# Kernel optimization log

Measured on AMD Instinct MI355X. Metric: run time of the kernel, lower is better.

The kernel has to match this reference:

```python
import jax, jax.numpy as jnp
import numpy as np

EPS_BN = 1e-5
EPS_NORM = 1e-12


def _l2norm_c(x):
    # F.normalize over channel dim (dim=1) of [n, d, h, w]
    n = jnp.sqrt(jnp.sum(x * x, axis=1, keepdims=True))
    return x / jnp.maximum(n, EPS_NORM)


def setup_inputs() -> dict:
    key = jax.random.key(0)
    ks = jax.random.split(key, 8)
    g, p, d, h, w = 64, 64, 512, 24, 8
    hw = h * w
    return {
        "gal_fea": jax.random.normal(ks[0], (g, d, h, w), dtype=jnp.float32),
        "prob_fea": jax.random.normal(ks[1], (p, d, h, w), dtype=jnp.float32),
        "bn_weight": jax.random.uniform(ks[2], (1,), dtype=jnp.float32) + 0.5,
        "bn_bias": jax.random.uniform(ks[3], (1,), dtype=jnp.float32) - 0.5,
        "bn_mean": jnp.zeros((1,), dtype=jnp.float32),
        "bn_var": jnp.ones((1,), dtype=jnp.float32),
        "fc_weight": jax.random.normal(ks[4], (1, 2 * hw), dtype=jnp.float32) * 0.05,
        "fc_bias": jax.random.normal(ks[5], (1,), dtype=jnp.float32) * 0.05,
        "lbn_weight": jax.random.uniform(ks[6], (1,), dtype=jnp.float32) + 0.5,
        "lbn_bias": jax.random.uniform(ks[7], (1,), dtype=jnp.float32) - 0.5,
        "lbn_mean": jnp.zeros((1,), dtype=jnp.float32),
        "lbn_var": jnp.ones((1,), dtype=jnp.float32),
    }


def reference(gal_fea, prob_fea, bn_weight, bn_bias, bn_mean, bn_var,
              fc_weight, fc_bias, lbn_weight, lbn_bias, lbn_mean, lbn_var):
    g, d, h, w = gal_fea.shape
    p = prob_fea.shape[0]
    hw = h * w

    # L2-normalize over channels, flatten spatial dims
    gal = _l2norm_c(gal_fea).reshape(g, d, hw)              # [g, d, j]
    ker = _l2norm_c(prob_fea).transpose(0, 2, 3, 1).reshape(p, hw, d)  # [p, i, d]

    # cosine-similarity cross-correlation: s[g,p,i,j] = <probe pos i, gallery pos j>
    s = jnp.einsum('pid,gdj->gpij', ker, gal)               # [g, p, hw, hw]

    # dual spatial max-pool: max over probe positions, max over gallery positions
    score = jnp.concatenate([s.max(axis=2), s.max(axis=3)], axis=-1)  # [g, p, 2*hw]

    # eval-mode BatchNorm1d(1): scalar affine broadcast over all elements
    score = (score - bn_mean) / jnp.sqrt(bn_var + EPS_BN) * bn_weight + bn_bias

    # fc: Linear(2*hw, 1)
    score = jnp.einsum('gpk,ok->gpo', score, fc_weight)[..., 0] + fc_bias[0]  # [g, p]

    # eval-mode logit BatchNorm1d(1): scalar affine
    score = (score - lbn_mean) / jnp.sqrt(lbn_var + EPS_BN) * lbn_weight + lbn_bias

    return jax.nn.sigmoid(score / 10.0)
```

## Files before the change

kernel.cpp:

```cpp
#include <hip/hip_runtime.h>

#define HW 192
#define DD 512
#define GG 64
#define PP 64
#define SLAB 98304

typedef __attribute__((ext_vector_type(4))) int intx4;

__device__ __forceinline__ unsigned int pk4(float a, float b, float c, float d) {
  int qa = (int)rintf(a), qb = (int)rintf(b), qc = (int)rintf(c), qd = (int)rintf(d);
  return (unsigned)(qa & 255) | ((unsigned)(qb & 255) << 8) |
         ((unsigned)(qc & 255) << 16) | ((unsigned)(qd & 255) << 24);
}

__global__ __launch_bounds__(512, 2) void norm_kernel(
    const float* __restrict__ gal, const float* __restrict__ prob,
    unsigned char* __restrict__ ws) {
  int b = blockIdx.x;
  int s = b / 12;
  int q = b - s * 12;
  const float* in = (s < GG) ? (gal + (size_t)s * DD * HW)
                             : (prob + (size_t)(s - GG) * DD * HW);
  unsigned char* out = ws + (size_t)s * SLAB;
  int pos0 = q * 16;
  int t = threadIdx.x;

  __shared__ float T[16][524];
  __shared__ float sqa[128][17];
  __shared__ float sq2[16][17];
  __shared__ float scl[16];

  {
    int cq = t >> 2;
    int quad = t & 3;
    float p0 = 0.f, p1 = 0.f, p2 = 0.f, p3 = 0.f;
#pragma unroll
    for (int cb = 0; cb < 4; ++cb) {
      int c = cb * 128 + cq;
      const float4 v = *(const float4*)(in + (size_t)c * HW + pos0 + quad * 4);
      T[quad * 4 + 0][c] = v.x;
      T[quad * 4 + 1][c] = v.y;
      T[quad * 4 + 2][c] = v.z;
      T[quad * 4 + 3][c] = v.w;
      p0 += v.x * v.x; p1 += v.y * v.y; p2 += v.z * v.z; p3 += v.w * v.w;
    }
    sqa[cq][quad * 4 + 0] = p0;
    sqa[cq][quad * 4 + 1] = p1;
    sqa[cq][quad * 4 + 2] = p2;
    sqa[cq][quad * 4 + 3] = p3;
  }
  __syncthreads();
  if (t < 256) {
    int g2 = t >> 4, pos = t & 15;
    float v = 0.f;
#pragma unroll
    for (int r = 0; r < 8; ++r) v += sqa[g2 * 8 + r][pos];
    sq2[g2][pos] = v;
  }
  __syncthreads();
  if (t < 16) {
    float v = 0.f;
#pragma unroll
    for (int r = 0; r < 16; ++r) v += sq2[r][t];
    scl[t] = 1.f / fmaxf(sqrtf(v), 1e-12f);
  }
  __syncthreads();

  {
    int kb2 = t >> 6;
    int lane = t & 63;
    int l4 = lane >> 4;
    int pos = lane & 15;
    float sc = scl[pos] * 127.f;
    int base = kb2 * 64 + l4 * 16;
    const float4 r0 = *(const float4*)&T[pos][base + 0];
    const float4 r1 = *(const float4*)&T[pos][base + 4];
    const float4 r2 = *(const float4*)&T[pos][base + 8];
    const float4 r3 = *(const float4*)&T[pos][base + 12];
    uint4 u;
    u.x = pk4(r0.x * sc, r0.y * sc, r0.z * sc, r0.w * sc);
    u.y = pk4(r1.x * sc, r1.y * sc, r1.z * sc, r1.w * sc);
    u.z = pk4(r2.x * sc, r2.y * sc, r2.z * sc, r2.w * sc);
    u.w = pk4(r3.x * sc, r3.y * sc, r3.z * sc, r3.w * sc);
    *(uint4*)(out + (size_t)kb2 * 12288 + (size_t)q * 1024 + (size_t)lane * 16) = u;
  }
}

__global__ __launch_bounds__(256, 2) void qaconv_gemm(
    const unsigned char* __restrict__ ws, const float* __restrict__ fcw,
    const float* __restrict__ bnw, const float* __restrict__ bnb,
    const float* __restrict__ bnm, const float* __restrict__ bnv,
    const float* __restrict__ fcb, const float* __restrict__ lw,
    const float* __restrict__ lb, const float* __restrict__ lm,
    const float* __restrict__ lv, float* __restrict__ out) {
  int bid = blockIdx.x;
  int sb = bid >> 6, li = bid & 63;
  int g = ((sb >> 3) << 3) + (li >> 3);
  int p = ((sb & 7) << 3) + (li & 7);
  const unsigned char* Bsrc = ws + (size_t)g * SLAB;
  const unsigned char* Asrc = ws + (size_t)(GG + p) * SLAB;

  __shared__ float colpart[2][HW];
  __shared__ float rowpart[2][HW];
  __shared__ float redbuf[4][2];

  int tid = threadIdx.x;
  int lane = tid & 63;
  int wave = tid >> 6;
  int wi = wave >> 1, wj = wave & 1;
  int l15 = lane & 15, l4 = lane >> 4;

  intx4 acc[6][6];
#pragma unroll
  for (int a = 0; a < 6; ++a)
#pragma unroll
    for (int c = 0; c < 6; ++c) acc[a][c] = (intx4){0, 0, 0, 0};

  const unsigned char* aP = Asrc + (size_t)(wi * 6) * 1024 + (size_t)lane * 16;
  const unsigned char* bP = Bsrc + (size_t)(wj * 6) * 1024 + (size_t)lane * 16;

#define LOADF(AD, BD, KB)                                                 \
  do {                                                                    \
    _Pragma("unroll") for (int it_ = 0; it_ < 6; ++it_) {                 \
      AD[it_] = *(const intx4*)(aP + (size_t)(KB)*12288 + it_ * 1024);    \
      BD[it_] = *(const intx4*)(bP + (size_t)(KB)*12288 + it_ * 1024);    \
    }                                                                     \
  } while (0)

#define MFMAB(AD, BD)                                                     \
  do {                                                                    \
    _Pragma("unroll") for (int jt_ = 0; jt_ < 6; ++jt_) {                 \
      intx4 bb = BD[jt_];                                                 \
      _Pragma("unroll") for (int it_ = 0; it_ < 6; ++it_)                 \
          acc[it_][jt_] = __builtin_amdgcn_mfma_i32_16x16x64_i8(          \
              AD[it_], bb, acc[it_][jt_], 0, 0, 0);                       \
    }                                                                     \
  } while (0)

  intx4 aC[6], bC[6], aN[6], bN[6];
  LOADF(aC, bC, 0);
#pragma unroll 1
  for (int kb2 = 0; kb2 < 8; kb2 += 2) {
    LOADF(aN, bN, kb2 + 1);
    MFMAB(aC, bC);
    if (kb2 < 6) LOADF(aC, bC, kb2 + 2);
    MFMAB(aN, bN);
  }
#undef LOADF
#undef MFMAB

  const float inv = 1.f / 16129.f;
  int cm[6];
  int rm[6][4];
#pragma unroll
  for (int jt = 0; jt < 6; ++jt) cm[jt] = -2147483647;
#pragma unroll
  for (int it = 0; it < 6; ++it)
#pragma unroll
    for (int r = 0; r < 4; ++r) rm[it][r] = -2147483647;
#pragma unroll
  for (int it = 0; it < 6; ++it)
#pragma unroll
    for (int jt = 0; jt < 6; ++jt)
#pragma unroll
      for (int r = 0; r < 4; ++r) {
        int v = acc[it][jt][r];
        cm[jt] = max(cm[jt], v);
        rm[it][r] = max(rm[it][r], v);
      }

#pragma unroll
  for (int jt = 0; jt < 6; ++jt) {
    int v = cm[jt];
    v = max(v, __shfl_xor(v, 16, 64));
    v = max(v, __shfl_xor(v, 32, 64));
    if (lane < 16) colpart[wi][wj * 96 + jt * 16 + lane] = (float)v * inv;
  }
#pragma unroll
  for (int it = 0; it < 6; ++it)
#pragma unroll
    for (int r = 0; r < 4; ++r) {
      int v = rm[it][r];
      v = max(v, __shfl_xor(v, 1, 64));
      v = max(v, __shfl_xor(v, 2, 64));
      v = max(v, __shfl_xor(v, 4, 64));
      v = max(v, __shfl_xor(v, 8, 64));
      if (l15 == 0) rowpart[wj][wi * 96 + it * 16 + l4 * 4 + r] = (float)v * inv;
    }
  __syncthreads();

  float part = 0.f, wpart = 0.f;
  if (tid < HW) {
    float cmax = fmaxf(colpart[0][tid], colpart[1][tid]);
    float rmax = fmaxf(rowpart[0][tid], rowpart[1][tid]);
    float w1 = fcw[tid], w2 = fcw[HW + tid];
    part = cmax * w1 + rmax * w2;
    wpart = w1 + w2;
  }
#pragma unroll
  for (int off = 32; off > 0; off >>= 1) {
    part += __shfl_down(part, off, 64);
    wpart += __shfl_down(wpart, off, 64);
  }
  if (lane == 0) { redbuf[wave][0] = part; redbuf[wave][1] = wpart; }
  __syncthreads();
  if (tid == 0) {
    float s = redbuf[0][0] + redbuf[1][0] + redbuf[2][0] + redbuf[3][0];
    float wsum = redbuf[0][1] + redbuf[1][1] + redbuf[2][1] + redbuf[3][1];
    float bnA = bnw[0] * rsqrtf(bnv[0] + 1e-5f);
    float bnB = bnb[0] - bnm[0] * bnA;
    float sc = bnA * s + bnB * wsum + fcb[0];
    float lA = lw[0] * rsqrtf(lv[0] + 1e-5f);
    sc = (sc - lm[0]) * lA + lb[0];
    out[g * PP + p] = 1.f / (1.f + __expf(-sc * 0.1f));
  }
}

extern "C" void kernel_launch(void* const* d_in, const int* in_sizes, int n_in,
                              void* d_out, int out_size, void* d_ws, size_t ws_size,
                              hipStream_t stream) {
  const float* gal  = (const float*)d_in[0];
  const float* prob = (const float*)d_in[1];
  const float* bnw  = (const float*)d_in[2];
  const float* bnb  = (const float*)d_in[3];
  const float* bnm  = (const float*)d_in[4];
  const float* bnv  = (const float*)d_in[5];
  const float* fcw  = (const float*)d_in[6];
  const float* fcb  = (const float*)d_in[7];
  const float* lw   = (const float*)d_in[8];
  const float* lb   = (const float*)d_in[9];
  const float* lm   = (const float*)d_in[10];
  const float* lv   = (const float*)d_in[11];
  unsigned char* ws = (unsigned char*)d_ws;
  float* out = (float*)d_out;

  hipLaunchKernelGGL(norm_kernel, dim3(1536), dim3(512), 0, stream, gal, prob, ws);
  hipLaunchKernelGGL(qaconv_gemm, dim3(GG * PP), dim3(256), 0, stream, ws, fcw,
                     bnw, bnb, bnm, bnv, fcb, lw, lb, lm, lv, out);
}
```

Before: 193.5 us.

## Restructure norm kernel to two-pass global reads without LDS transpose

The normalization/quantization kernel now gives each block 64 spatial positions (384 blocks of 256 threads instead of 1536 of 512). It first computes per-position sums of squares with coalesced scalar loads, then rereads the input from global memory (likely served by cache) to scale, quantize and pack int8 directly, removing the large LDS transpose buffer and its multi-stage reduction. In exchange the input is read twice and the second pass uses strided 64-byte-per-row access, and far fewer blocks are launched.

```diff
diff --git a/kernel.cpp b/kernel.cpp
--- a/kernel.cpp
+++ b/kernel.cpp
@@ -14,76 +14,60 @@
          ((unsigned)(qc & 255) << 16) | ((unsigned)(qd & 255) << 24);
 }
 
-__global__ __launch_bounds__(512, 2) void norm_kernel(
+__global__ __launch_bounds__(256, 4) void norm_kernel(
     const float* __restrict__ gal, const float* __restrict__ prob,
     unsigned char* __restrict__ ws) {
   int b = blockIdx.x;
-  int s = b / 12;
-  int q = b - s * 12;
+  int s = b / 3;
+  int h = b - s * 3;
   const float* in = (s < GG) ? (gal + (size_t)s * DD * HW)
                              : (prob + (size_t)(s - GG) * DD * HW);
   unsigned char* out = ws + (size_t)s * SLAB;
-  int pos0 = q * 16;
   int t = threadIdx.x;
-
-  __shared__ float T[16][524];
-  __shared__ float sqa[128][17];
-  __shared__ float sq2[16][17];
-  __shared__ float scl[16];
+  int lane = t & 63;
+  int wave = t >> 6;
+
+  __shared__ float ssqA[4][64];
+  __shared__ float sc127[64];
 
   {
-    int cq = t >> 2;
-    int quad = t & 3;
-    float p0 = 0.f, p1 = 0.f, p2 = 0.f, p3 = 0.f;
-#pragma unroll
-    for (int cb = 0; cb < 4; ++cb) {
-      int c = cb * 128 + cq;
-      const float4 v = *(const float4*)(in + (size_t)c * HW + pos0 + quad * 4);
-      T[quad * 4 + 0][c] = v.x;
-      T[quad * 4 + 1][c] = v.y;
-      T[quad * 4 + 2][c] = v.z;
-      T[quad * 4 + 3][c] = v.w;
-      p0 += v.x * v.x; p1 += v.y * v.y; p2 += v.z * v.z; p3 += v.w * v.w;
+    const float* base = in + (size_t)(wave * 128) * HW + h * 64 + lane;
+    float ssq = 0.f;
+#pragma unroll 8
+    for (int k = 0; k < 128; ++k) {
+      float v = base[(size_t)k * HW];
+      ssq += v * v;
     }
-    sqa[cq][quad * 4 + 0] = p0;
-    sqa[cq][quad * 4 + 1] = p1;
-    sqa[cq][quad * 4 + 2] = p2;
-    sqa[cq][quad * 4 + 3] = p3;
-  }
-  __syncthreads();
-  if (t < 256) {
-    int g2 = t >> 4, pos = t & 15;
-    float v = 0.f;
-#pragma unroll
-    for (int r = 0; r < 8; ++r) v += sqa[g2 * 8 + r][pos];
-    sq2[g2][pos] = v;
-  }
-  __syncthreads();
-  if (t < 16) {
-    float v = 0.f;
-#pragma unroll
-    for (int r = 0; r < 16; ++r) v += sq2[r][t];
-    scl[t] = 1.f / fmaxf(sqrtf(v), 1e-12f);
+    ssqA[wave][lane] = ssq;
+  }
+  __syncthreads();
+  if (t < 64) {
+    float v = ssqA[0][t] + ssqA[1][t] + ssqA[2][t] + ssqA[3][t];
+    sc127[t] = 127.f / fmaxf(sqrtf(v), 1e-12f);
   }
   __syncthreads();
 
   {
-    int kb2 = t >> 6;
-    int lane = t & 63;
-    int l4 = lane >> 4;
-    int pos = lane & 15;
-    float sc = scl[pos] * 127.f;
-    int base = kb2 * 64 + l4 * 16;
-    const float4 r0 = *(const float4*)&T[pos][base + 0];
-    const float4 r1 = *(const float4*)&T[pos][base + 4];
-    const float4 r2 = *(const float4*)&T[pos][base + 8];
-    const float4 r3 = *(const float4*)&T[pos][base + 12];
-    uint4 u;
-    u.x = pk4(r0.x * sc, r0.y * sc, r0.z * sc, r0.w * sc);
-    u.y = pk4(r1.x * sc, r1.y * sc, r1.z * sc, r1.w * sc);
-    u.z = pk4(r2.x * sc, r2.y * sc, r2.z * sc, r2.w * sc);
-    u.w = pk4(r3.x * sc, r3.y * sc, r3.z * sc, r3.w * sc);
-    *(uint4*)(out + (size_t)kb2 * 12288 + (size_t)q * 1024 + (size_t)lane * 16) = u;
+    int lpos = t & 15, l4 = (t >> 4) & 3, qloc = t >> 6;
+    int posl = qloc * 16 + lpos;
+    int q = h * 4 + qloc;
+    float sc = sc127[posl];
+    const float* pbase = in + (size_t)h * 64 + posl;
+    uint4* o = (uint4*)out;
+#pragma unroll
+    for (int kb2 = 0; kb2 < 8; ++kb2) {
+      int c0 = kb2 * 64 + l4 * 16;
+      const float* cp = pbase + (size_t)c0 * HW;
+      float v[16];
+#pragma unroll
+      for (int j = 0; j < 16; ++j) v[j] = cp[(size_t)j * HW] * sc;
+      uint4 u;
+      u.x = pk4(v[0], v[1], v[2], v[3]);
+      u.y = pk4(v[4], v[5], v[6], v[7]);
+      u.z = pk4(v[8], v[9], v[10], v[11]);
+      u.w = pk4(v[12], v[13], v[14], v[15]);
+      o[kb2 * 768 + q * 64 + l4 * 16 + lpos] = u;
+    }
   }
 }
 
@@ -235,7 +219,7 @@
   unsigned char* ws = (unsigned char*)d_ws;
   float* out = (float*)d_out;
 
-  hipLaunchKernelGGL(norm_kernel, dim3(1536), dim3(512), 0, stream, gal, prob, ws);
+  hipLaunchKernelGGL(norm_kernel, dim3(384), dim3(256), 0, stream, gal, prob, ws);
   hipLaunchKernelGGL(qaconv_gemm, dim3(GG * PP), dim3(256), 0, stream, ws, fcw,
                      bnw, bnb, bnm, bnv, fcb, lw, lb, lm, lv, out);
 }
```

Measured after the change: 195.6 us. Within noise of the previous version (+1.1%).
